# Optimization experiments

Measured on AMD Instinct MI355X. Metric: run time of the kernel, lower is better.

## Reference

```python
import jax, jax.numpy as jnp
import numpy as np
from jax import lax

# dims
BATCH, SEQ, DMODEL = 2, 2048, 1024
EXPAND, HEADDIM, DSTATE, DCONV, MLP_INNER = 2, 64, 64, 4, 4096
DIN = EXPAND * DMODEL            # 2048
NH = DIN // HEADDIM              # 32 heads
CONV_DIM = DIN + 2 * DSTATE      # x, B, C go through the depthwise conv
DPROJ = 2 * DIN + 2 * DSTATE + NH  # z, xBC, dt
EPS = 1e-5


def rmsnorm(x, w):
    return x * lax.rsqrt(jnp.mean(x * x, axis=-1, keepdims=True) + EPS) * w


def setup_inputs() -> dict:
    key = jax.random.key(0)
    ks = jax.random.split(key, 12)
    n = lambda i, shape, scale: jax.random.normal(ks[i], shape, jnp.float32) * scale
    return {
        "hidden_tokens": n(0, (BATCH, SEQ, DMODEL), 1.0),
        "W_in": n(1, (DMODEL, DPROJ), DMODEL ** -0.5),
        "conv_w": n(2, (CONV_DIM, DCONV), 0.2),
        "conv_b": jnp.zeros((CONV_DIM,), jnp.float32),
        "dt_bias": jax.random.uniform(ks[3], (NH,), jnp.float32, -4.0, -1.0),
        "A_log": jnp.log(jax.random.uniform(ks[4], (NH,), jnp.float32, 1.0, 16.0)),
        "D_param": n(5, (NH,), 1.0),
        "norm_w": jnp.ones((DIN,), jnp.float32),
        "W_out": n(6, (DIN, DMODEL), DIN ** -0.5),
        "rms_w": jnp.ones((DMODEL,), jnp.float32),
        "mlp_w1": n(7, (DMODEL, MLP_INNER), DMODEL ** -0.5),
        "mlp_b1": jnp.zeros((MLP_INNER,), jnp.float32),
        "mlp_w2": n(8, (MLP_INNER, DMODEL), MLP_INNER ** -0.5),
        "mlp_b2": jnp.zeros((DMODEL,), jnp.float32),
    }


def _mamba2(x, W_in, conv_w, conv_b, dt_bias, A_log, D_param, norm_w, W_out):
    b, l, _ = x.shape
    zxbcdt = x @ W_in                                   # (b,l,DPROJ)
    z = zxbcdt[..., :DIN]
    xBC = zxbcdt[..., DIN:DIN + CONV_DIM]
    dt = zxbcdt[..., DIN + CONV_DIM:]                   # (b,l,NH)

    # depthwise causal conv1d over sequence
    xt = jnp.pad(xBC, ((0, 0), (DCONV - 1, 0), (0, 0))).transpose(0, 2, 1)  # (b,c,l+pad)
    conv = lax.conv_general_dilated(xt, conv_w[:, None, :], (1,), "VALID",
                                    feature_group_count=CONV_DIM,
                                    dimension_numbers=("NCH", "OIH", "NCH"))
    xBC = jax.nn.silu(conv.transpose(0, 2, 1) + conv_b)  # (b,l,CONV_DIM)

    xs = xBC[..., :DIN].reshape(b, l, NH, HEADDIM)       # (b,l,h,p)
    Bc = xBC[..., DIN:DIN + DSTATE]                      # (b,l,n), ngroups=1
    Cc = xBC[..., DIN + DSTATE:]                         # (b,l,n)

    dt = jax.nn.softplus(dt + dt_bias)                   # (b,l,h)
    A = -jnp.exp(A_log)                                  # (h,)
    dA = jnp.exp(dt * A)                                 # (b,l,h)
    dtx = dt[..., None] * xs                             # (b,l,h,p)

    def step(h, inp):
        dA_t, dtx_t, B_t, C_t = inp                      # (b,h),(b,h,p),(b,n),(b,n)
        h = dA_t[..., None, None] * h + dtx_t[..., None] * B_t[:, None, None, :]
        y = jnp.einsum("bhpn,bn->bhp", h, C_t)
        return h, y

    h0 = jnp.zeros((b, NH, HEADDIM, DSTATE), x.dtype)
    _, ys = lax.scan(step, h0, (dA.transpose(1, 0, 2), dtx.transpose(1, 0, 2, 3),
                                Bc.transpose(1, 0, 2), Cc.transpose(1, 0, 2)))
    y = ys.transpose(1, 0, 2, 3) + D_param[None, None, :, None] * xs  # (b,l,h,p)
    y = y.reshape(b, l, DIN)
    y = rmsnorm(y * jax.nn.silu(z), norm_w)              # gated RMSNorm
    return y @ W_out


def reference(hidden_tokens, W_in, conv_w, conv_b, dt_bias, A_log, D_param,
              norm_w, W_out, rms_w, mlp_w1, mlp_b1, mlp_w2, mlp_b2):
    h = hidden_tokens + _mamba2(hidden_tokens, W_in, conv_w, conv_b, dt_bias,
                                A_log, D_param, norm_w, W_out)
    hn = rmsnorm(h, rms_w)
    mlp = jax.nn.silu(hn @ mlp_w1 + mlp_b1) @ mlp_w2 + mlp_b2
    return h + mlp
```

## Files before the change

### kernel.cpp

```cpp
#include <hip/hip_runtime.h>
#include <hip/hip_bf16.h>
#include <cstdint>
#include <cstddef>

#define BATCH 2
#define SEQ 2048
#define DMODEL 1024
#define DIN 2048
#define NH 32
#define HEADDIM 64
#define DSTATE 64
#define DCONV 4
#define CONV_DIM (DIN + 2 * DSTATE)
#define DPROJ (2 * DIN + 2 * DSTATE + NH)
#define MLP_INNER 4096
#define TOKENS (BATCH * SEQ)
#define EPS 1e-5f
#define Q 64
#define NCHUNK (SEQ / Q)
#define NCH (BATCH * NCHUNK * NH)
#define LSTR 72
#define NPAD_IN 4352

typedef __attribute__((ext_vector_type(8))) short short8;
typedef __attribute__((ext_vector_type(8))) __bf16 bf16x8;
typedef __attribute__((ext_vector_type(4))) float f32x4;

__device__ inline short f2bf(float f) {
    unsigned u = __builtin_bit_cast(unsigned, f);
    u = (u + 0x7FFFu + ((u >> 16) & 1u)) >> 16;
    return (short)u;
}
__device__ inline float bf2f(short s) {
    unsigned u = ((unsigned)(unsigned short)s) << 16;
    return __builtin_bit_cast(float, u);
}
__device__ inline float silu_f(float x) { return x / (1.f + __expf(-x)); }

__device__ inline bf16x8 ld_frag(const short* p) {
    short8 s = *(const short8*)p;
    return __builtin_bit_cast(bf16x8, s);
}

__device__ inline void glds16(const short* g, short* l) {
    __builtin_amdgcn_global_load_lds(
        (const __attribute__((address_space(1))) void*)g,
        (__attribute__((address_space(3))) void*)l, 16, 0, 0);
}

template <int MODE, int KT>
__global__ __launch_bounds__(256, (KT == 32) ? 4 : 2) void gemm_bf16_kernel(
    const short* __restrict__ A, const short* __restrict__ BT,
    void* __restrict__ Cout, const float* __restrict__ bias,
    const float* __restrict__ res, int M, int N, int K)
{
    const int tid  = threadIdx.x;
    const int wid  = tid >> 6;
    const int lane = tid & 63;
    const int lm   = lane & 15;
    const int lg   = lane >> 4;

    const int nb  = gridDim.x * gridDim.y;
    const int bid = blockIdx.y * gridDim.x + blockIdx.x;
    const int per = nb >> 3;
    const int nid = (bid & 7) * per + (bid >> 3);
    const int m0  = (nid / gridDim.x) * 128;
    const int n0  = (nid % gridDim.x) * 128;

    __shared__ __attribute__((aligned(16))) short Al0[128 * KT];
    __shared__ __attribute__((aligned(16))) short Al1[128 * KT];
    __shared__ __attribute__((aligned(16))) short Bl0[128 * KT];
    __shared__ __attribute__((aligned(16))) short Bl1[128 * KT];

    f32x4 acc[4][4];
#pragma unroll
    for (int i = 0; i < 4; ++i)
#pragma unroll
        for (int j = 0; j < 4; ++j) acc[i][j] = {0.f, 0.f, 0.f, 0.f};

    const int wm = (wid >> 1) * 64;
    const int wn = (wid & 1) * 64;

    constexpr int lpr = KT / 8;
    constexpr int rpi = 64 / lpr;
    constexpr int nin = 32 / rpi;
    const int srow = lane / lpr;
    const int scb  = (lane % lpr) ^ (srow & (lpr - 1));
    const int scol = scb * 8;
    const short* Ag = A  + (size_t)(m0 + wid * 32 + srow) * K + scol;
    const short* Bg = BT + (size_t)(n0 + wid * 32 + srow) * K + scol;
    const int woff = wid * 32 * KT;

    const int niter = K / KT;
    {
#pragma unroll
        for (int j = 0; j < nin; ++j) {
            glds16(Ag + (size_t)j * rpi * K, Al0 + woff + j * 512);
            glds16(Bg + (size_t)j * rpi * K, Bl0 + woff + j * 512);
        }
    }

    for (int i = 0; i < niter; ++i) {
        __syncthreads();
        const short* Ac = (i & 1) ? Al1 : Al0;
        const short* Bc = (i & 1) ? Bl1 : Bl0;
        if (i + 1 < niter) {
            int kt = (i + 1) * KT;
            short* al = ((i & 1) ? Al0 : Al1) + woff;
            short* bl = ((i & 1) ? Bl0 : Bl1) + woff;
#pragma unroll
            for (int j = 0; j < nin; ++j) {
                glds16(Ag + kt + (size_t)j * rpi * K, al + j * 512);
                glds16(Bg + kt + (size_t)j * rpi * K, bl + j * 512);
            }
        }

#pragma unroll
        for (int sub = 0; sub < KT / 32; ++sub) {
            const int cb = sub * 4 + lg;
            bf16x8 af[4], bf[4];
#pragma unroll
            for (int ii = 0; ii < 4; ++ii) {
                int ar = wm + ii * 16 + lm;
                af[ii] = ld_frag(&Ac[ar * KT + ((cb ^ (ar & (lpr - 1))) * 8)]);
            }
#pragma unroll
            for (int j = 0; j < 4; ++j) {
                int br = wn + j * 16 + lm;
                bf[j] = ld_frag(&Bc[br * KT + ((cb ^ (br & (lpr - 1))) * 8)]);
            }
#pragma unroll
            for (int ii = 0; ii < 4; ++ii)
#pragma unroll
                for (int j = 0; j < 4; ++j)
                    acc[ii][j] = __builtin_amdgcn_mfma_f32_16x16x32_bf16(af[ii], bf[j], acc[ii][j], 0, 0, 0);
        }
    }

#pragma unroll
    for (int i = 0; i < 4; ++i) {
#pragma unroll
        for (int j = 0; j < 4; ++j) {
            int col = n0 + wn + j * 16 + lm;
            if (col >= N) continue;
            float bv = (MODE == 1 || MODE == 2) ? bias[col] : 0.f;
#pragma unroll
            for (int r = 0; r < 4; ++r) {
                int row = m0 + wm + i * 16 + lg * 4 + r;
                float v = acc[i][j][r];
                if (MODE == 1) {
                    ((short*)Cout)[(size_t)row * N + col] = f2bf(silu_f(v + bv));
                } else if (MODE == 4) {
                    ((short*)Cout)[(size_t)row * N + col] = f2bf(v);
                } else {
                    if (MODE == 2) v = v + bv + res[(size_t)row * N + col];
                    if (MODE == 3) v = v + res[(size_t)row * N + col];
                    ((float*)Cout)[(size_t)row * N + col] = v;
                }
            }
        }
    }
}

__global__ __launch_bounds__(256) void cvt_kernel(
    const float* __restrict__ src, short* __restrict__ dst, int n4)
{
    int i = (blockIdx.x * 256 + threadIdx.x);
    if (i >= n4) return;
    f32x4 v = *(const f32x4*)(src + (size_t)i * 4);
    short4 o;
    o.x = f2bf(v.x); o.y = f2bf(v.y); o.z = f2bf(v.z); o.w = f2bf(v.w);
    *(short4*)(dst + (size_t)i * 4) = o;
}

__global__ __launch_bounds__(256) void transpose_kernel(
    const float* __restrict__ src, short* __restrict__ dst, int K, int N)
{
    __shared__ float t[32][33];
    int bx = blockIdx.x, by = blockIdx.y;
    int col = threadIdx.x & 31, row8 = threadIdx.x >> 5;
    int gn = bx * 32 + col;
#pragma unroll
    for (int r = 0; r < 4; ++r) {
        int gk = by * 32 + row8 + r * 8;
        t[row8 + r * 8][col] = (gn < N) ? src[(size_t)gk * N + gn] : 0.f;
    }
    __syncthreads();
#pragma unroll
    for (int r = 0; r < 4; ++r) {
        int n = bx * 32 + row8 + r * 8;
        dst[(size_t)n * K + by * 32 + col] = f2bf(t[col][row8 + r * 8]);
    }
}

#define CTOK 8
__global__ __launch_bounds__(256) void conv_kernel(
    const short* __restrict__ zx, const float* __restrict__ cw,
    const float* __restrict__ cb, short* __restrict__ xBCc)
{
    int c4 = blockIdx.y * 256 + threadIdx.x;
    if (c4 >= CONV_DIM / 4) return;
    int c  = c4 * 4;
    int m0 = blockIdx.x * CTOK;
    int l0 = m0 & (SEQ - 1);

    const short* base = zx + (size_t)m0 * DPROJ + DIN + c;
    f32x4 win[CTOK + 3];
#pragma unroll
    for (int j = 0; j < CTOK + 3; ++j) {
        int off = j - 3;
        if (l0 + off >= 0) {
            short4 sv = *(const short4*)(base + (ptrdiff_t)off * DPROJ);
            win[j] = {bf2f(sv.x), bf2f(sv.y), bf2f(sv.z), bf2f(sv.w)};
        } else {
            win[j] = {0.f, 0.f, 0.f, 0.f};
        }
    }
    f32x4 w0 = *(const f32x4*)(cw + (c + 0) * DCONV);
    f32x4 w1 = *(const f32x4*)(cw + (c + 1) * DCONV);
    f32x4 w2 = *(const f32x4*)(cw + (c + 2) * DCONV);
    f32x4 w3 = *(const f32x4*)(cw + (c + 3) * DCONV);
    f32x4 bb = *(const f32x4*)(cb + c);

    short* outp = xBCc + (size_t)m0 * CONV_DIM + c;
#pragma unroll
    for (int t = 0; t < CTOK; ++t) {
        f32x4 a = {bb.x, bb.y, bb.z, bb.w};
#pragma unroll
        for (int j = 0; j < DCONV; ++j) {
            f32x4 v = win[t + j];
            a.x += v.x * w0[j];
            a.y += v.y * w1[j];
            a.z += v.z * w2[j];
            a.w += v.w * w3[j];
        }
        short4 o;
        o.x = f2bf(silu_f(a.x)); o.y = f2bf(silu_f(a.y));
        o.z = f2bf(silu_f(a.z)); o.w = f2bf(silu_f(a.w));
        *(short4*)(outp + (size_t)t * CONV_DIM) = o;
    }
}

__global__ __launch_bounds__(256) void dt_kernel(
    const short* __restrict__ zx, const float* __restrict__ dt_bias,
    const float* __restrict__ A_log, float* __restrict__ dtb, float* __restrict__ ldab)
{
    int idx = blockIdx.x * 256 + threadIdx.x;
    if (idx >= TOKENS * NH) return;
    int hh = idx & (NH - 1);
    int m  = idx >> 5;
    float v  = bf2f(zx[(size_t)m * DPROJ + DIN + CONV_DIM + hh]) + dt_bias[hh];
    float dt = (v > 20.f) ? v : log1pf(__expf(v));
    dtb[idx]  = dt;
    ldab[idx] = -__expf(A_log[hh]) * dt;
}

__global__ __launch_bounds__(256) void chunk_kernel(
    const short* __restrict__ xBCc, const float* __restrict__ dtb,
    const float* __restrict__ ldab, float* __restrict__ ybuf,
    float* __restrict__ Sbuf, float* __restrict__ cumdecay)
{
    int bid = blockIdx.x;
    int h = bid & 31, c = (bid >> 5) & 31, b = bid >> 10;
    int m0 = b * SEQ + c * Q;
    int tid = threadIdx.x;
    int wid = tid >> 6, lane = tid & 63, lm = lane & 15, lg = lane >> 4;

    __shared__ __attribute__((aligned(16))) short Cc[64 * LSTR];
    __shared__ __attribute__((aligned(16))) short Bb[64 * LSTR];
    __shared__ __attribute__((aligned(16))) short BwT[64 * LSTR];
    __shared__ __attribute__((aligned(16))) short Xt[64 * LSTR];
    __shared__ __attribute__((aligned(16))) short Mm[64 * LSTR];
    __shared__ float Lc[64], dtv[64];

    if (tid < 64) {
        int s = tid;
        size_t ix = (size_t)(m0 + s) * NH + h;
        float ld = ldab[ix];
        float dt = dtb[ix];
        float v = ld;
#pragma unroll
        for (int off = 1; off < 64; off <<= 1) {
            float o = __shfl_up(v, off);
            if (s >= off) v += o;
        }
        Lc[s] = v;
        dtv[s] = dt;
        cumdecay[(size_t)bid * 64 + s] = __expf(v);
    }
    {
        int row = tid >> 2, c0 = (tid & 3) * 16;
        const short* pB = xBCc + (size_t)(m0 + row) * CONV_DIM + DIN;
#pragma unroll
        for (int u = 0; u < 2; ++u) {
            short8 vb = *(const short8*)(pB + c0 + 8 * u);
            short8 vc = *(const short8*)(pB + DSTATE + c0 + 8 * u);
            *(short8*)&Bb[row * LSTR + c0 + 8 * u] = vb;
            *(short8*)&Cc[row * LSTR + c0 + 8 * u] = vc;
        }
    }
    __syncthreads();
    {
        int s = tid >> 2, c0 = (tid & 3) * 16;
        float w = dtv[s];
        float w2 = __expf(Lc[63] - Lc[s]);
        const short* pX = xBCc + (size_t)(m0 + s) * CONV_DIM + h * HEADDIM;
#pragma unroll
        for (int u = 0; u < 4; ++u) {
            short4 v = *(const short4*)(pX + c0 + 4 * u);
            Xt[(c0 + 4 * u + 0) * LSTR + s] = f2bf(bf2f(v.x) * w);
            Xt[(c0 + 4 * u + 1) * LSTR + s] = f2bf(bf2f(v.y) * w);
            Xt[(c0 + 4 * u + 2) * LSTR + s] = f2bf(bf2f(v.z) * w);
            Xt[(c0 + 4 * u + 3) * LSTR + s] = f2bf(bf2f(v.w) * w);
            short4 sb = *(short4*)&Bb[s * LSTR + c0 + 4 * u];
            BwT[(c0 + 4 * u + 0) * LSTR + s] = f2bf(bf2f(sb.x) * w2);
            BwT[(c0 + 4 * u + 1) * LSTR + s] = f2bf(bf2f(sb.y) * w2);
            BwT[(c0 + 4 * u + 2) * LSTR + s] = f2bf(bf2f(sb.z) * w2);
            BwT[(c0 + 4 * u + 3) * LSTR + s] = f2bf(bf2f(sb.w) * w2);
        }
    }
    __syncthreads();

    {
        bf16x8 af[2];
#pragma unroll
        for (int kk = 0; kk < 2; ++kk)
            af[kk] = ld_frag(&Cc[(wid * 16 + lm) * LSTR + kk * 32 + lg * 8]);
#pragma unroll
        for (int j = 0; j < 4; ++j) {
            f32x4 acc = {0.f, 0.f, 0.f, 0.f};
#pragma unroll
            for (int kk = 0; kk < 2; ++kk) {
                bf16x8 bf = ld_frag(&Bb[(j * 16 + lm) * LSTR + kk * 32 + lg * 8]);
                acc = __builtin_amdgcn_mfma_f32_16x16x32_bf16(af[kk], bf, acc, 0, 0, 0);
            }
            int s = j * 16 + lm;
            float Ls = Lc[s];
#pragma unroll
            for (int r = 0; r < 4; ++r) {
                int t = wid * 16 + lg * 4 + r;
                float val = (s <= t) ? acc[r] * __expf(Lc[t] - Ls) : 0.f;
                Mm[t * LSTR + s] = f2bf(val);
            }
        }
    }
    __syncthreads();

    {
        bf16x8 am[2], aw[2];
#pragma unroll
        for (int kk = 0; kk < 2; ++kk) {
            am[kk] = ld_frag(&Mm[(wid * 16 + lm) * LSTR + kk * 32 + lg * 8]);
            aw[kk] = ld_frag(&BwT[(wid * 16 + lm) * LSTR + kk * 32 + lg * 8]);
        }
#pragma unroll
        for (int j = 0; j < 4; ++j) {
            f32x4 a1 = {0.f, 0.f, 0.f, 0.f};
            f32x4 a2 = {0.f, 0.f, 0.f, 0.f};
#pragma unroll
            for (int kk = 0; kk < 2; ++kk) {
                bf16x8 bx = ld_frag(&Xt[(j * 16 + lm) * LSTR + kk * 32 + lg * 8]);
                a1 = __builtin_amdgcn_mfma_f32_16x16x32_bf16(am[kk], bx, a1, 0, 0, 0);
                a2 = __builtin_amdgcn_mfma_f32_16x16x32_bf16(aw[kk], bx, a2, 0, 0, 0);
            }
            int p = j * 16 + lm;
#pragma unroll
            for (int r = 0; r < 4; ++r) {
                int t = wid * 16 + lg * 4 + r;
                ybuf[(size_t)(m0 + t) * DIN + h * HEADDIM + p] = a1[r];
                Sbuf[(size_t)bid * 4096 + t * 64 + p] = a2[r];
            }
        }
    }
}

__global__ __launch_bounds__(256) void state_kernel(
    float* __restrict__ SH, const float* __restrict__ cumdecay)
{
    int bh = blockIdx.x;
    int b = bh >> 5, h = bh & 31;
    int tid = threadIdx.x;
    f32x4 H[4];
#pragma unroll
    for (int u = 0; u < 4; ++u) H[u] = {0.f, 0.f, 0.f, 0.f};
    for (int c = 0; c < NCHUNK; ++c) {
        int cid = (b * NCHUNK + c) * NH + h;
        size_t base = (size_t)cid * 4096 + (size_t)tid * 16;
        float cd = cumdecay[(size_t)cid * 64 + 63];
        f32x4 s[4];
#pragma unroll
        for (int u = 0; u < 4; ++u) s[u] = *(const f32x4*)(SH + base + u * 4);
#pragma unroll
        for (int u = 0; u < 4; ++u) *(f32x4*)(SH + base + u * 4) = H[u];
#pragma unroll
        for (int u = 0; u < 4; ++u) {
            H[u].x = cd * H[u].x + s[u].x;
            H[u].y = cd * H[u].y + s[u].y;
            H[u].z = cd * H[u].z + s[u].z;
            H[u].w = cd * H[u].w + s[u].w;
        }
    }
}

__global__ __launch_bounds__(256) void inter_kernel(
    const short* __restrict__ xBCc, const float* __restrict__ Hin,
    const float* __restrict__ cumdecay, float* __restrict__ ybuf)
{
    int bid = blockIdx.x;
    int h = bid & 31, c = (bid >> 5) & 31, b = bid >> 10;
    int m0 = b * SEQ + c * Q;
    int tid = threadIdx.x;
    int wid = tid >> 6, lane = tid & 63, lm = lane & 15, lg = lane >> 4;

    __shared__ __attribute__((aligned(16))) short Cc[64 * LSTR];
    __shared__ __attribute__((aligned(16))) short HT[64 * LSTR];
    __shared__ float eLc[64];

    if (tid < 64) eLc[tid] = cumdecay[(size_t)bid * 64 + tid];
    {
        int row = tid >> 2, c0 = (tid & 3) * 16;
        const short* pC = xBCc + (size_t)(m0 + row) * CONV_DIM + DIN + DSTATE;
#pragma unroll
        for (int u = 0; u < 2; ++u) {
            short8 vc = *(const short8*)(pC + c0 + 8 * u);
            *(short8*)&Cc[row * LSTR + c0 + 8 * u] = vc;
        }
        const float* pH = Hin + (size_t)bid * 4096 + row * 64;
#pragma unroll
        for (int u = 0; u < 4; ++u) {
            f32x4 vh = *(const f32x4*)(pH + c0 + 4 * u);
            HT[(c0 + 4 * u + 0) * LSTR + row] = f2bf(vh.x);
            HT[(c0 + 4 * u + 1) * LSTR + row] = f2bf(vh.y);
            HT[(c0 + 4 * u + 2) * LSTR + row] = f2bf(vh.z);
            HT[(c0 + 4 * u + 3) * LSTR + row] = f2bf(vh.w);
        }
    }
    __syncthreads();

    bf16x8 af[2];
#pragma unroll
    for (int kk = 0; kk < 2; ++kk)
        af[kk] = ld_frag(&Cc[(wid * 16 + lm) * LSTR + kk * 32 + lg * 8]);
#pragma unroll
    for (int j = 0; j < 4; ++j) {
        f32x4 acc = {0.f, 0.f, 0.f, 0.f};
#pragma unroll
        for (int kk = 0; kk < 2; ++kk) {
            bf16x8 bh_ = ld_frag(&HT[(j * 16 + lm) * LSTR + kk * 32 + lg * 8]);
            acc = __builtin_amdgcn_mfma_f32_16x16x32_bf16(af[kk], bh_, acc, 0, 0, 0);
        }
        int p = j * 16 + lm;
#pragma unroll
        for (int r = 0; r < 4; ++r) {
            int t = wid * 16 + lg * 4 + r;
            size_t ya = (size_t)(m0 + t) * DIN + h * HEADDIM + p;
            ybuf[ya] += eLc[t] * acc[r];
        }
    }
}

__global__ __launch_bounds__(256) void norm1_kernel(
    const short* __restrict__ zx, const short* __restrict__ xBCc,
    const float* __restrict__ Dp, const float* __restrict__ y,
    short* __restrict__ ybf, const float* __restrict__ w)
{
    int m = blockIdx.x;
    int t = threadIdx.x;
    const short* zr = zx + (size_t)m * DPROJ;
    const short* xr = xBCc + (size_t)m * CONV_DIM;
    const float* yr = y + (size_t)m * DIN;
    float vals[8];
    float ss = 0.f;
#pragma unroll
    for (int j = 0; j < 8; ++j) {
        int i = j * 256 + t;
        float v = (yr[i] + Dp[i >> 6] * bf2f(xr[i])) * silu_f(bf2f(zr[i]));
        vals[j] = v;
        ss += v * v;
    }
#pragma unroll
    for (int o = 32; o >= 1; o >>= 1) ss += __shfl_xor(ss, o);
    __shared__ float wsum[4];
    if ((t & 63) == 0) wsum[t >> 6] = ss;
    __syncthreads();
    float tot = wsum[0] + wsum[1] + wsum[2] + wsum[3];
    float scale = rsqrtf(tot / (float)DIN + EPS);
#pragma unroll
    for (int j = 0; j < 8; ++j) {
        int i = j * 256 + t;
        ybf[(size_t)m * DIN + i] = f2bf(vals[j] * scale * w[i]);
    }
}

__global__ __launch_bounds__(256) void norm2_kernel(
    const float* __restrict__ hb, short* __restrict__ hnbf, const float* __restrict__ w)
{
    int m = blockIdx.x;
    int t = threadIdx.x;
    const float* hr = hb + (size_t)m * DMODEL;
    float vals[4];
    float ss = 0.f;
#pragma unroll
    for (int j = 0; j < 4; ++j) {
        int i = j * 256 + t;
        float v = hr[i];
        vals[j] = v;
        ss += v * v;
    }
#pragma unroll
    for (int o = 32; o >= 1; o >>= 1) ss += __shfl_xor(ss, o);
    __shared__ float wsum[4];
    if ((t & 63) == 0) wsum[t >> 6] = ss;
    __syncthreads();
    float tot = wsum[0] + wsum[1] + wsum[2] + wsum[3];
    float scale = rsqrtf(tot / (float)DMODEL + EPS);
#pragma unroll
    for (int j = 0; j < 4; ++j) {
        int i = j * 256 + t;
        hnbf[(size_t)m * DMODEL + i] = f2bf(vals[j] * scale * w[i]);
    }
}

extern "C" void kernel_launch(void* const* d_in, const int* in_sizes, int n_in,
                              void* d_out, int out_size, void* d_ws, size_t ws_size,
                              hipStream_t stream) {
    const float* x       = (const float*)d_in[0];
    const float* W_in    = (const float*)d_in[1];
    const float* conv_w  = (const float*)d_in[2];
    const float* conv_b  = (const float*)d_in[3];
    const float* dt_bias = (const float*)d_in[4];
    const float* A_log   = (const float*)d_in[5];
    const float* D_param = (const float*)d_in[6];
    const float* norm_w  = (const float*)d_in[7];
    const float* W_out   = (const float*)d_in[8];
    const float* rms_w   = (const float*)d_in[9];
    const float* mlp_w1  = (const float*)d_in[10];
    const float* mlp_b1  = (const float*)d_in[11];
    const float* mlp_w2  = (const float*)d_in[12];
    const float* mlp_b2  = (const float*)d_in[13];
    float* out = (float*)d_out;

    float* ws       = (float*)d_ws;
    float* zxf      = ws;
    float* xBCf     = zxf + (size_t)TOKENS * DPROJ;
    float* dtb      = xBCf + (size_t)TOKENS * CONV_DIM;
    float* ldab     = dtb + (size_t)TOKENS * NH;
    float* cumdecay = ldab + (size_t)TOKENS * NH;
    float* ybuf     = cumdecay + (size_t)TOKENS * NH;
    float* SH       = ybuf + (size_t)TOKENS * DIN;
    float* bfarea   = SH + (size_t)NCH * 4096;

    short* zxb   = (short*)zxf;
    short* xBCb  = (short*)xBCf;
    short* xbf   = (short*)ybuf;
    short* midbf = (short*)ybuf;
    float* hbuf  = SH;
    short* hnbf  = (short*)(SH + (size_t)TOKENS * DMODEL);

    short* ybf   = (short*)bfarea;
    short* WinT  = ybf + (size_t)TOKENS * DIN;
    short* WoutT = WinT + (size_t)NPAD_IN * DMODEL;
    short* w1T   = WoutT + (size_t)DMODEL * DIN;
    short* w2T   = w1T + (size_t)MLP_INNER * DMODEL;

    dim3 blk(256);

    cvt_kernel<<<dim3(TOKENS * DMODEL / 4 / 256), blk, 0, stream>>>(x, xbf, TOKENS * DMODEL / 4);
    transpose_kernel<<<dim3(NPAD_IN / 32, DMODEL / 32), blk, 0, stream>>>(W_in, WinT, DMODEL, DPROJ);
    transpose_kernel<<<dim3(DMODEL / 32, DIN / 32), blk, 0, stream>>>(W_out, WoutT, DIN, DMODEL);
    transpose_kernel<<<dim3(MLP_INNER / 32, DMODEL / 32), blk, 0, stream>>>(mlp_w1, w1T, DMODEL, MLP_INNER);
    transpose_kernel<<<dim3(DMODEL / 32, MLP_INNER / 32), blk, 0, stream>>>(mlp_w2, w2T, MLP_INNER, DMODEL);

    gemm_bf16_kernel<4, 32><<<dim3(NPAD_IN / 128, TOKENS / 128), blk, 0, stream>>>(
        xbf, WinT, zxb, nullptr, nullptr, TOKENS, DPROJ, DMODEL);
    conv_kernel<<<dim3(TOKENS / CTOK, (CONV_DIM / 4 + 255) / 256), blk, 0, stream>>>(
        zxb, conv_w, conv_b, xBCb);
    dt_kernel<<<dim3(TOKENS * NH / 256), blk, 0, stream>>>(zxb, dt_bias, A_log, dtb, ldab);
    chunk_kernel<<<dim3(NCH), blk, 0, stream>>>(xBCb, dtb, ldab, ybuf, SH, cumdecay);
    state_kernel<<<dim3(BATCH * NH), blk, 0, stream>>>(SH, cumdecay);
    inter_kernel<<<dim3(NCH), blk, 0, stream>>>(xBCb, SH, cumdecay, ybuf);
    norm1_kernel<<<dim3(TOKENS), blk, 0, stream>>>(zxb, xBCb, D_param, ybuf, ybf, norm_w);
    gemm_bf16_kernel<3, 64><<<dim3(DMODEL / 128, TOKENS / 128), blk, 0, stream>>>(
        ybf, WoutT, hbuf, nullptr, x, TOKENS, DMODEL, DIN);
    norm2_kernel<<<dim3(TOKENS), blk, 0, stream>>>(hbuf, hnbf, rms_w);
    gemm_bf16_kernel<1, 32><<<dim3(MLP_INNER / 128, TOKENS / 128), blk, 0, stream>>>(
        hnbf, w1T, midbf, mlp_b1, nullptr, TOKENS, MLP_INNER, DMODEL);
    gemm_bf16_kernel<2, 64><<<dim3(DMODEL / 128, TOKENS / 128), blk, 0, stream>>>(
        midbf, w2T, out, mlp_b2, hbuf, TOKENS, DMODEL, MLP_INNER);
}
```

Before: 424.9 us.

## Add 256x256-tile 512-thread GEMM kernel for in-projection and MLP up-projection

Adds a new bf16 MFMA GEMM kernel with 256x256 output tiles, 8 waves and double-buffered LDS staging via global_load_lds, with split-K half-tiles interleaved with MFMAs and setprio hints. It replaces the 128x128 kernel for the W_in projection and the mlp_w1 GEMM. The larger tiles raise arithmetic intensity and cut global traffic per FLOP. In exchange the grid shrinks (e.g. 17x16 and 16x16 blocks), which lowers occupancy and may leave CUs underused on a 256-CU part. Register pressure also rises with 32 accumulators per thread.

```diff
diff --git a/kernel.cpp b/kernel.cpp
--- a/kernel.cpp
+++ b/kernel.cpp
@@ -48,6 +48,134 @@
         (__attribute__((address_space(3))) void*)l, 16, 0, 0);
 }
 
+template <int MODE>
+__global__ __launch_bounds__(512, 2) void gemm256_kernel(
+    const short* __restrict__ A, const short* __restrict__ BT,
+    void* __restrict__ Cout, const float* __restrict__ bias,
+    int M, int N, int K)
+{
+    const int tid  = threadIdx.x;
+    const int wid  = tid >> 6;
+    const int lane = tid & 63;
+    const int lm   = lane & 15;
+    const int lg   = lane >> 4;
+    const int wm   = (wid >> 2) * 128;
+    const int wn   = (wid & 3) * 64;
+
+    const int nb  = gridDim.x * gridDim.y;
+    const int bid = blockIdx.y * gridDim.x + blockIdx.x;
+    const int per = nb >> 3;
+    const int nid = (bid & 7) * per + (bid >> 3);
+    const int m0  = (nid / gridDim.x) * 256;
+    const int n0  = (nid % gridDim.x) * 256;
+
+    __shared__ __attribute__((aligned(16))) short Ab[2][2][256 * 32];
+    __shared__ __attribute__((aligned(16))) short Bb[2][2][256 * 32];
+
+    f32x4 acc[8][4];
+#pragma unroll
+    for (int i = 0; i < 8; ++i)
+#pragma unroll
+        for (int j = 0; j < 4; ++j) acc[i][j] = {0.f, 0.f, 0.f, 0.f};
+
+    const int q   = tid & 7;
+    const int jj  = (tid >> 3) & 3;
+    const int win = tid >> 5;
+    const int r0  = win * 8 + q;
+    const short* Asrc = A  + (size_t)(m0 + r0) * K + jj * 8;
+    const short* Bsrc = BT + (size_t)(n0 + r0) * K + jj * 8;
+    const size_t rstep = (size_t)128 * K;
+    const int dst = wid * 512;
+
+#define STAGE(src, buf) do {                  \
+        glds16((src), (buf) + dst);           \
+        glds16((src) + rstep, (buf) + 4096 + dst); } while (0)
+
+    bf16x8 af[8], bfr[4];
+
+#define READS(As, Bs) do {                                                     \
+        _Pragma("unroll")                                                      \
+        for (int fi = 0; fi < 8; ++fi) {                                       \
+            int rr = wm + fi * 16 + lm;                                        \
+            af[fi] = ld_frag((As) + ((rr >> 3) << 8) + ((rr & 7) << 3) + (lg << 6)); \
+        }                                                                      \
+        _Pragma("unroll")                                                      \
+        for (int fj = 0; fj < 4; ++fj) {                                       \
+            int rr = wn + fj * 16 + lm;                                        \
+            bfr[fj] = ld_frag((Bs) + ((rr >> 3) << 8) + ((rr & 7) << 3) + (lg << 6)); \
+        }                                                                      \
+    } while (0)
+
+#define MFMAP(FJA) do {                                                        \
+        __builtin_amdgcn_s_setprio(1);                                         \
+        _Pragma("unroll")                                                      \
+        for (int fi = 0; fi < 8; ++fi) {                                       \
+            acc[fi][FJA]     = __builtin_amdgcn_mfma_f32_16x16x32_bf16(af[fi], bfr[FJA],     acc[fi][FJA],     0, 0, 0); \
+            acc[fi][FJA + 1] = __builtin_amdgcn_mfma_f32_16x16x32_bf16(af[fi], bfr[FJA + 1], acc[fi][FJA + 1], 0, 0, 0); \
+        }                                                                      \
+        __builtin_amdgcn_s_setprio(0); } while (0)
+
+    const int NT = K >> 6;
+
+    STAGE(Asrc,      &Ab[0][0][0]);
+    STAGE(Bsrc,      &Bb[0][0][0]);
+    STAGE(Asrc + 32, &Ab[0][1][0]);
+    STAGE(Bsrc + 32, &Bb[0][1][0]);
+
+    for (int t = 0; t < NT - 1; ++t) {
+        const int bi = t & 1, bn = bi ^ 1;
+        const int kn = (t + 1) << 6;
+        STAGE(Asrc + kn, &Ab[bn][0][0]);
+        asm volatile("s_waitcnt vmcnt(6)\n\ts_barrier" ::: "memory");
+        READS(&Ab[bi][0][0], &Bb[bi][0][0]);
+        MFMAP(0);
+        STAGE(Bsrc + kn, &Bb[bn][0][0]);
+        asm volatile("s_barrier" ::: "memory");
+        MFMAP(2);
+        STAGE(Asrc + kn + 32, &Ab[bn][1][0]);
+        asm volatile("s_waitcnt vmcnt(6)\n\ts_barrier" ::: "memory");
+        READS(&Ab[bi][1][0], &Bb[bi][1][0]);
+        MFMAP(0);
+        STAGE(Bsrc + kn + 32, &Bb[bn][1][0]);
+        asm volatile("s_barrier" ::: "memory");
+        MFMAP(2);
+    }
+    {
+        const int bi = (NT - 1) & 1;
+        asm volatile("s_waitcnt vmcnt(4)\n\ts_barrier" ::: "memory");
+        READS(&Ab[bi][0][0], &Bb[bi][0][0]);
+        MFMAP(0);
+        asm volatile("s_barrier" ::: "memory");
+        MFMAP(2);
+        asm volatile("s_waitcnt vmcnt(0)\n\ts_barrier" ::: "memory");
+        READS(&Ab[bi][1][0], &Bb[bi][1][0]);
+        MFMAP(0);
+        asm volatile("s_barrier" ::: "memory");
+        MFMAP(2);
+    }
+#undef STAGE
+#undef READS
+#undef MFMAP
+
+#pragma unroll
+    for (int fj = 0; fj < 4; ++fj) {
+        int col = n0 + wn + fj * 16 + lm;
+        if (col < N) {
+            float bv = (MODE == 1) ? bias[col] : 0.f;
+#pragma unroll
+            for (int fi = 0; fi < 8; ++fi) {
+#pragma unroll
+                for (int r = 0; r < 4; ++r) {
+                    int row = m0 + wm + fi * 16 + lg * 4 + r;
+                    float v = acc[fi][fj][r];
+                    if (MODE == 1) v = silu_f(v + bv);
+                    ((short*)Cout)[(size_t)row * N + col] = f2bf(v);
+                }
+            }
+        }
+    }
+}
+
 template <int MODE, int KT>
 __global__ __launch_bounds__(256, (KT == 32) ? 4 : 2) void gemm_bf16_kernel(
     const short* __restrict__ A, const short* __restrict__ BT,
@@ -564,6 +692,7 @@
     short* w2T   = w1T + (size_t)MLP_INNER * DMODEL;
 
     dim3 blk(256);
+    dim3 blk2(512);
 
     cvt_kernel<<<dim3(TOKENS * DMODEL / 4 / 256), blk, 0, stream>>>(x, xbf, TOKENS * DMODEL / 4);
     transpose_kernel<<<dim3(NPAD_IN / 32, DMODEL / 32), blk, 0, stream>>>(W_in, WinT, DMODEL, DPROJ);
@@ -571,8 +700,8 @@
     transpose_kernel<<<dim3(MLP_INNER / 32, DMODEL / 32), blk, 0, stream>>>(mlp_w1, w1T, DMODEL, MLP_INNER);
     transpose_kernel<<<dim3(DMODEL / 32, MLP_INNER / 32), blk, 0, stream>>>(mlp_w2, w2T, MLP_INNER, DMODEL);
 
-    gemm_bf16_kernel<4, 32><<<dim3(NPAD_IN / 128, TOKENS / 128), blk, 0, stream>>>(
-        xbf, WinT, zxb, nullptr, nullptr, TOKENS, DPROJ, DMODEL);
+    gemm256_kernel<4><<<dim3(NPAD_IN / 256, TOKENS / 256), blk2, 0, stream>>>(
+        xbf, WinT, zxb, nullptr, TOKENS, DPROJ, DMODEL);
     conv_kernel<<<dim3(TOKENS / CTOK, (CONV_DIM / 4 + 255) / 256), blk, 0, stream>>>(
         zxb, conv_w, conv_b, xBCb);
     dt_kernel<<<dim3(TOKENS * NH / 256), blk, 0, stream>>>(zxb, dt_bias, A_log, dtb, ldab);
@@ -583,8 +712,8 @@
     gemm_bf16_kernel<3, 64><<<dim3(DMODEL / 128, TOKENS / 128), blk, 0, stream>>>(
         ybf, WoutT, hbuf, nullptr, x, TOKENS, DMODEL, DIN);
     norm2_kernel<<<dim3(TOKENS), blk, 0, stream>>>(hbuf, hnbf, rms_w);
-    gemm_bf16_kernel<1, 32><<<dim3(MLP_INNER / 128, TOKENS / 128), blk, 0, stream>>>(
-        hnbf, w1T, midbf, mlp_b1, nullptr, TOKENS, MLP_INNER, DMODEL);
+    gemm256_kernel<1><<<dim3(MLP_INNER / 256, TOKENS / 256), blk2, 0, stream>>>(
+        hnbf, w1T, midbf, mlp_b1, TOKENS, MLP_INNER, DMODEL);
     gemm_bf16_kernel<2, 64><<<dim3(DMODEL / 128, TOKENS / 128), blk, 0, stream>>>(
         midbf, w2T, out, mlp_b2, hbuf, TOKENS, DMODEL, MLP_INNER);
 }
```

After: 464.1 us. 1.09x slower.
